# Kernel tuning notes

Measured on AMD Instinct MI355X. Metric: run time of the kernel, lower is better.

Reference implementation:

```python
import jax, jax.numpy as jnp
import numpy as np

GROUPS = 16
N_HEADS = 4
EPS = 1e-6


def setup_inputs() -> dict:
    key = jax.random.key(0)
    ks = jax.random.split(key, 7)
    N, C, D, H, W = 2, 256, 16, 16, 16
    x = jax.random.normal(ks[0], (N, C, D, H, W), jnp.float32)
    gn_scale = 1.0 + 0.02 * jax.random.normal(ks[1], (C,), jnp.float32)
    gn_bias = 0.02 * jax.random.normal(ks[2], (C,), jnp.float32)
    w_qkv = jax.random.normal(ks[3], (3 * C, C), jnp.float32) / np.sqrt(C).astype(np.float32)
    b_qkv = 0.02 * jax.random.normal(ks[4], (3 * C,), jnp.float32)
    # NOTE: original zero-inits w_out/b_out (zero_module); we use random values
    # so the kernel-correctness baseline is non-trivial. Same math.
    w_out = jax.random.normal(ks[5], (C, C), jnp.float32) / np.sqrt(C).astype(np.float32)
    b_out = 0.02 * jax.random.normal(ks[6], (C,), jnp.float32)
    return {"x": x, "gn_scale": gn_scale, "gn_bias": gn_bias,
            "w_qkv": w_qkv, "b_qkv": b_qkv, "w_out": w_out, "b_out": b_out}


def reference(x, gn_scale, gn_bias, w_qkv, b_qkv, w_out, b_out):
    N, C, D, H, W = x.shape
    L = D * H * W
    xf = x.reshape(N, C, L)
    # GroupNorm(16 groups, eps=1e-6, affine)
    xg = xf.reshape(N, GROUPS, C // GROUPS, L)
    mu = xg.mean(axis=(2, 3), keepdims=True)
    var = xg.var(axis=(2, 3), keepdims=True)
    xn = ((xg - mu) * jax.lax.rsqrt(var + EPS)).reshape(N, C, L)
    xn = xn * gn_scale[None, :, None] + gn_bias[None, :, None]
    # 1x1x1 Conv3d == channel matmul
    qkv = jnp.einsum('oc,ncl->nol', w_qkv, xn) + b_qkv[None, :, None]  # [N,3C,L]
    ch = C // N_HEADS
    qkv = qkv.reshape(N, 3, N_HEADS, ch, L)  # channel layout: (qkvs, head, ch)
    q, k, v = qkv[:, 0], qkv[:, 1], qkv[:, 2]  # each [N,heads,ch,L]
    scale = 1.0 / np.sqrt(np.sqrt(ch)).astype(np.float32)
    w = jnp.einsum('nhct,nhcs->nhts', q * scale, k * scale)  # [N,heads,L,L]
    w = jax.nn.softmax(w, axis=-1)
    a = jnp.einsum('nhts,nhcs->nhct', w, v).reshape(N, C, L)
    y = jnp.einsum('oc,ncl->nol', w_out, a) + b_out[None, :, None]
    return x + y.reshape(N, C, D, H, W)
```

## Files before the change

kernel.cpp:

```cpp
#include <hip/hip_runtime.h>

#define NB 2
#define CCH 256
#define LL 4096
#define NGRP 16
#define NHD 4
#define CHD 64
#define QR 768
#define SPLIT 4
#define TBLK 256

typedef __attribute__((ext_vector_type(8))) short short8;
typedef __attribute__((ext_vector_type(4))) float f32x4;
typedef __attribute__((ext_vector_type(4))) unsigned int uint32x4;

#define OFF_GP 64
#define OFF_BP 4224
#define OFF_WQ 5824
#define OFF_WO 202432
#define OFF_QT 235200
#define OFF_KT 1283776
#define OFF_V  2332352
#define OFF_PO 3380928
#define OFF_L  7575232
#define OFF_XT OFF_PO
#define OFF_AT OFF_QT

#define KSCALE 0.1803368801111204f

__device__ __forceinline__ unsigned short f2bf(float f) {
    unsigned int u = __builtin_bit_cast(unsigned int, f);
    u += 0x7fffu + ((u >> 16) & 1u);
    return (unsigned short)(u >> 16);
}
__device__ __forceinline__ float bf2f(unsigned short s) {
    unsigned int u = ((unsigned int)s) << 16;
    return __builtin_bit_cast(float, u);
}
__device__ __forceinline__ unsigned int cvtpk(float lo, float hi) {
    unsigned int r;
    asm("v_cvt_pk_bf16_f32 %0, %1, %2" : "=v"(r) : "v"(lo), "v"(hi));
    return r;
}

__device__ __forceinline__ short8 build_pf(const f32x4 s_lo, const f32x4 s_hi) {
    unsigned int a0 = cvtpk(s_lo[0], s_lo[1]);
    unsigned int b0 = cvtpk(s_hi[0], s_hi[1]);
    unsigned int a1 = cvtpk(s_lo[2], s_lo[3]);
    unsigned int b1 = cvtpk(s_hi[2], s_hi[3]);
    asm("v_permlane32_swap_b32 %0, %1" : "+v"(a0), "+v"(b0));
    asm("v_permlane16_swap_b32 %0, %1" : "+v"(a0), "+v"(b0));
    asm("v_permlane32_swap_b32 %0, %1" : "+v"(a1), "+v"(b1));
    asm("v_permlane16_swap_b32 %0, %1" : "+v"(a1), "+v"(b1));
    uint32x4 w = {a0, a1, b0, b1};
    return __builtin_bit_cast(short8, w);
}

__device__ __forceinline__ void stage_tile(unsigned short* lt,
                                           const unsigned short* src,
                                           int srcStride, int tid) {
    #pragma unroll
    for (int p = 0; p < 4; p++) {
        const int r  = p * 16 + (tid >> 4);
        const int cb = (tid & 15) * 2;
        const unsigned short* s = src + (size_t)r * srcStride + cb * 8;
        short8 a = *(const short8*)(s);
        short8 b = *(const short8*)(s + 8);
        char* d = (char*)lt + r * 512;
        *(short8*)(d + (((cb    ) ^ (r & 15)) << 4)) = a;
        *(short8*)(d + (((cb + 1) ^ (r & 15)) << 4)) = b;
    }
}
__device__ __forceinline__ short8 ldsfrag(const unsigned short* lt, int row, int ch) {
    return *(const short8*)((const char*)lt + row * 512 + ((ch ^ (row & 15)) << 4));
}

__global__ __launch_bounds__(256)
void k_xtgn(const float* __restrict__ x, unsigned short* __restrict__ xt,
            float* __restrict__ ws) {
    const int l0 = blockIdx.x * 64, c0 = blockIdx.y * 64, n = blockIdx.z;
    __shared__ __align__(16) unsigned short lt[64 * 64];
    __shared__ float red[2][4][4];
    const int tid = threadIdx.x;
    const int cl = tid >> 4;
    const int ll = (tid & 15) << 2;
    float s1[4], s2[4];
    #pragma unroll
    for (int cc = 0; cc < 4; cc++) {
        const int c = cl + cc * 16;
        float4 v = *(const float4*)(x + (size_t)(n * CCH + c0 + c) * LL + l0 + ll);
        s1[cc] = (v.x + v.y) + (v.z + v.w);
        s2[cc] = (v.x * v.x + v.y * v.y) + (v.z * v.z + v.w * v.w);
        const float vv[4] = {v.x, v.y, v.z, v.w};
        #pragma unroll
        for (int j = 0; j < 4; j++) {
            const int l = ll + j;
            const int byte = l * 128 + ((((c >> 3) ^ (l & 7)) << 4) | ((c & 7) * 2));
            *(unsigned short*)((char*)lt + byte) = f2bf(vv[j]);
        }
    }
    #pragma unroll
    for (int cc = 0; cc < 4; cc++)
        #pragma unroll
        for (int off = 32; off; off >>= 1) {
            s1[cc] += __shfl_down(s1[cc], off);
            s2[cc] += __shfl_down(s2[cc], off);
        }
    if ((tid & 63) == 0) {
        const int w = tid >> 6;
        #pragma unroll
        for (int cc = 0; cc < 4; cc++) { red[0][w][cc] = s1[cc]; red[1][w][cc] = s2[cc]; }
    }
    __syncthreads();
    if (tid < 4) {
        const float a = red[0][0][tid] + red[0][1][tid] + red[0][2][tid] + red[0][3][tid];
        const float b = red[1][0][tid] + red[1][1][tid] + red[1][2][tid] + red[1][3][tid];
        const int g = n * NGRP + (c0 >> 4) + tid;
        ws[OFF_GP + (g * 64 + blockIdx.x) * 2]     = a;
        ws[OFF_GP + (g * 64 + blockIdx.x) * 2 + 1] = b;
    }
    const int lr = tid >> 2;
    const int ch = (tid & 3) << 4;
    unsigned short* dst = xt + ((size_t)n * LL + l0 + lr) * CCH + c0 + ch;
    const int b0 = lr * 128 + ((((ch >> 3)    ) ^ (lr & 7)) << 4);
    const int b1 = lr * 128 + ((((ch >> 3) + 1) ^ (lr & 7)) << 4);
    *(short8*)dst       = *(const short8*)((char*)lt + b0);
    *(short8*)(dst + 8) = *(const short8*)((char*)lt + b1);
}

__device__ __forceinline__ void load_stats(const float* __restrict__ ws,
                                           float* smu, float* srs) {
    if (threadIdx.x < 32) {
        float s1 = 0.f, s2 = 0.f;
        #pragma unroll 8
        for (int i = 0; i < 64; i++) {
            s1 += ws[OFF_GP + (threadIdx.x * 64 + i) * 2];
            s2 += ws[OFF_GP + (threadIdx.x * 64 + i) * 2 + 1];
        }
        const float inv = 1.f / (float)(16 * LL);
        float m = s1 * inv;
        float var = s2 * inv - m * m;
        smu[threadIdx.x] = m;
        srs[threadIdx.x] = rsqrtf(var + 1e-6f);
    }
    __syncthreads();
}

__global__ __launch_bounds__(256)
void k_bpw(const float* __restrict__ w_qkv, const float* __restrict__ w_out,
           const float* __restrict__ b_qkv, const float* __restrict__ gn_scale,
           const float* __restrict__ gn_bias, float* __restrict__ ws,
           unsigned short* __restrict__ wq, unsigned short* __restrict__ wo) {
    __shared__ float smu[32], srs[32];
    load_stats(ws, smu, srs);
    if (blockIdx.x < 448) {
        const int e = (blockIdx.x * 256 + threadIdx.x) * 4;
        if (e < NB * QR * CCH) {
            const int n = (e >= QR * CCH) ? 1 : 0;
            const int r = e - n * QR * CCH;
            const int o = r >> 8, c = r & 255;
            float4 w  = *(const float4*)(w_qkv + (size_t)o * CCH + c);
            float4 gs = *(const float4*)(gn_scale + c);
            const float rs = srs[n * NGRP + (c >> 4)];
            const float sc = (o < 256 ? KSCALE : 1.0f) * rs;
            ushort4 u;
            u.x = f2bf(w.x * gs.x * sc); u.y = f2bf(w.y * gs.y * sc);
            u.z = f2bf(w.z * gs.z * sc); u.w = f2bf(w.w * gs.w * sc);
            *(ushort4*)(wq + (size_t)n * QR * CCH + r) = u;
        } else {
            const int r = e - NB * QR * CCH;
            float4 w = *(const float4*)(w_out + r);
            ushort4 u;
            u.x = f2bf(w.x); u.y = f2bf(w.y); u.z = f2bf(w.z); u.w = f2bf(w.w);
            *(ushort4*)(wo + r) = u;
        }
    } else {
        const int oi = (blockIdx.x - 448) * 32 + (threadIdx.x >> 3);
        const int j  = threadIdx.x & 7;
        const int n = (oi >= QR) ? 1 : 0;
        const int o = oi - n * QR;
        const float* wr = w_qkv + (size_t)o * CCH + j * 32;
        const float* gsr = gn_scale + j * 32;
        const float* gbr = gn_bias + j * 32;
        float s = 0.f;
        #pragma unroll
        for (int c = 0; c < 32; c += 4) {
            float4 w  = *(const float4*)(wr + c);
            float4 gs = *(const float4*)(gsr + c);
            float4 gb = *(const float4*)(gbr + c);
            const int gidx = n * NGRP + ((j * 32 + c) >> 4);
            const float mu = smu[gidx], rs = srs[gidx];
            s += w.x * (gb.x - mu * rs * gs.x) + w.y * (gb.y - mu * rs * gs.y)
               + w.z * (gb.z - mu * rs * gs.z) + w.w * (gb.w - mu * rs * gs.w);
        }
        s += __shfl_down(s, 4);
        s += __shfl_down(s, 2);
        s += __shfl_down(s, 1);
        if (j == 0) ws[OFF_BP + oi] = (b_qkv[o] + s) * (o < 256 ? KSCALE : 1.0f);
    }
}

__global__ __launch_bounds__(256)
void k_qkv(const unsigned short* __restrict__ wq, const float* __restrict__ bp,
           const unsigned short* __restrict__ xt,
           unsigned short* __restrict__ qT, unsigned short* __restrict__ kT,
           unsigned short* __restrict__ vv) {
    const int l0 = blockIdx.x * 64, o0 = blockIdx.y * 64, n = blockIdx.z;
    const int tid = threadIdx.x, w = tid >> 6, r16 = tid & 15, g = (tid & 63) >> 4;
    __shared__ __align__(16) unsigned short lt[64 * 256];
    const unsigned short* xb = xt + (size_t)n * LL * CCH;
    const unsigned short* wb = wq + (size_t)n * QR * CCH;
    const bool isv = (o0 >= 512);

    stage_tile(lt, isv ? (xb + (size_t)l0 * CCH) : (wb + (size_t)o0 * CCH), CCH, tid);
    __syncthreads();

    f32x4 acc[4];
    #pragma unroll
    for (int i = 0; i < 4; i++) acc[i] = (f32x4){0.f, 0.f, 0.f, 0.f};

    if (!isv) {
        const unsigned short* xr = xb + (size_t)(l0 + w * 16 + r16) * CCH + g * 8;
        for (int kk = 0; kk < 8; kk++) {
            short8 xf = *(const short8*)(xr + kk * 32);
            #pragma unroll
            for (int af = 0; af < 4; af++) {
                short8 wf = ldsfrag(lt, af * 16 + r16, kk * 4 + g);
                acc[af] = __builtin_amdgcn_mfma_f32_16x16x32_bf16(wf, xf, acc[af], 0, 0, 0);
            }
        }
        const bool isq = (o0 < 256);
        const int h = (o0 >> 6) & 3;
        unsigned short* tb = (isq ? qT : kT) + ((size_t)n * NHD + h) * LL * CHD;
        const int t = l0 + w * 16 + r16;
        #pragma unroll
        for (int af = 0; af < 4; af++) {
            float4 bb = *(const float4*)(bp + n * QR + o0 + af * 16 + g * 4);
            ushort4 u;
            u.x = f2bf(acc[af][0] + bb.x); u.y = f2bf(acc[af][1] + bb.y);
            u.z = f2bf(acc[af][2] + bb.z); u.w = f2bf(acc[af][3] + bb.w);
            *(ushort4*)(tb + (size_t)t * CHD + af * 16 + g * 4) = u;
        }
    } else {
        const unsigned short* wr = wb + (size_t)(o0 + w * 16 + r16) * CCH + g * 8;
        for (int kk = 0; kk < 8; kk++) {
            short8 wf = *(const short8*)(wr + kk * 32);
            #pragma unroll
            for (int lb = 0; lb < 4; lb++) {
                short8 xf = ldsfrag(lt, lb * 16 + r16, kk * 4 + g);
                acc[lb] = __builtin_amdgcn_mfma_f32_16x16x32_bf16(xf, wf, acc[lb], 0, 0, 0);
            }
        }
        const int h = (o0 - 512) >> 6;
        const int o = o0 + w * 16 + r16;
        const float bb = bp[n * QR + o];
        unsigned short* vb = vv + ((size_t)n * NHD + h) * CHD * LL + (size_t)(o & 63) * LL;
        #pragma unroll
        for (int lb = 0; lb < 4; lb++) {
            ushort4 u;
            u.x = f2bf(acc[lb][0] + bb); u.y = f2bf(acc[lb][1] + bb);
            u.z = f2bf(acc[lb][2] + bb); u.w = f2bf(acc[lb][3] + bb);
            *(ushort4*)(vb + l0 + lb * 16 + g * 4) = u;
        }
    }
}

__global__ __launch_bounds__(256, 2)
void k_attn(const unsigned short* __restrict__ qT,
            const unsigned short* __restrict__ kT,
            const unsigned short* __restrict__ vv,
            unsigned short* __restrict__ po, float* __restrict__ pl) {
    const int t0 = blockIdx.x * TBLK;
    const int h  = blockIdx.y;
    const int n  = blockIdx.z >> 2;
    const int sp = blockIdx.z & 3;
    const int tid = threadIdx.x;
    const int w = tid >> 6, l = tid & 63, r16 = l & 15, g = l >> 4;

    const size_t nh = (size_t)n * NHD + h;
    const unsigned short* qb = qT + nh * LL * CHD;
    const unsigned short* kb = kT + nh * LL * CHD;
    const unsigned short* vb = vv + nh * CHD * LL;
    const int s_beg = sp * (LL / SPLIT);

    __shared__ __align__(16) unsigned short kvs[2][2][64 * 64];

    const int srow = tid >> 2;
    const int ss0  = (tid & 3) << 1;
    const unsigned short* ksrc = kb + (size_t)(s_beg + srow) * CHD + ss0 * 8;
    const unsigned short* vsrc = vb + (size_t)srow * LL + s_beg + ss0 * 8;
    char* base0 = (char*)&kvs[0][0][0];
    const int kd0 = srow * 128 + (((ss0    ) ^ (srow & 7)) << 4);
    const int kd1 = srow * 128 + (((ss0 + 1) ^ (srow & 7)) << 4);

    const int tw = t0 + w * 64;
    const int jk0 = ((g    ) ^ (r16 & 7)) << 4;
    const int jk1 = ((4 + g) ^ (r16 & 7)) << 4;

    short8 qf[4][2];
    #pragma unroll
    for (int qg = 0; qg < 4; qg++) {
        const unsigned short* qr = qb + (size_t)(tw + qg * 16 + r16) * CHD + g * 8;
        qf[qg][0] = *(const short8*)(qr);
        qf[qg][1] = *(const short8*)(qr + 32);
    }

    f32x4 oacc[4][4];
    #pragma unroll
    for (int qg = 0; qg < 4; qg++)
        #pragma unroll
        for (int cb = 0; cb < 4; cb++) oacc[qg][cb] = (f32x4){0.f, 0.f, 0.f, 0.f};
    float lsum[4] = {0.f, 0.f, 0.f, 0.f};

    const int NIT = (LL / SPLIT) / 64;

    short8 kr0 = *(const short8*)(ksrc);
    short8 kr1 = *(const short8*)(ksrc + 8);
    short8 vr0 = *(const short8*)(vsrc);
    short8 vr1 = *(const short8*)(vsrc + 8);
    *(short8*)(base0 + kd0) = kr0;
    *(short8*)(base0 + kd1) = kr1;
    *(short8*)(base0 + 8192 + kd0) = vr0;
    *(short8*)(base0 + 8192 + kd1) = vr1;
    const unsigned short* kpf = ksrc + 64 * CHD;
    const unsigned short* vpf = vsrc + 64;
    kr0 = *(const short8*)(kpf);
    kr1 = *(const short8*)(kpf + 8);
    vr0 = *(const short8*)(vpf);
    vr1 = *(const short8*)(vpf + 8);
    __syncthreads();

    int cur = 0;
    for (int it = 0; it < NIT; it++) {
        const char* kB = base0 + cur * 16384;
        const char* vB = kB + 8192;

        short8 kf0[4], kf1[4];
        #pragma unroll
        for (int sb = 0; sb < 4; sb++) {
            const int rb = (16 * sb + r16) * 128;
            kf0[sb] = *(const short8*)(kB + rb + jk0);
            kf1[sb] = *(const short8*)(kB + rb + jk1);
        }
        if (it + 1 < NIT) {
            char* kdn = base0 + (cur ^ 1) * 16384;
            *(short8*)(kdn + kd0) = kr0;
            *(short8*)(kdn + kd1) = kr1;
            *(short8*)(kdn + 8192 + kd0) = vr0;
            *(short8*)(kdn + 8192 + kd1) = vr1;
        }
        if (it + 2 < NIT) {
            kpf += 64 * CHD;
            vpf += 64;
            kr0 = *(const short8*)(kpf);
            kr1 = *(const short8*)(kpf + 8);
            vr0 = *(const short8*)(vpf);
            vr1 = *(const short8*)(vpf + 8);
        }

        short8 pf[4][2];
        #pragma unroll
        for (int qg = 0; qg < 4; qg++) {
            f32x4 sa[4];
            #pragma unroll
            for (int sb = 0; sb < 4; sb++) {
                f32x4 z = (f32x4){0.f, 0.f, 0.f, 0.f};
                z = __builtin_amdgcn_mfma_f32_16x16x32_bf16(kf0[sb], qf[qg][0], z, 0, 0, 0);
                sa[sb] = __builtin_amdgcn_mfma_f32_16x16x32_bf16(kf1[sb], qf[qg][1], z, 0, 0, 0);
            }
            float rs0 = 0.f, rs1 = 0.f;
            #pragma unroll
            for (int sb = 0; sb < 4; sb++) {
                float p0 = __builtin_amdgcn_exp2f(sa[sb][0]);
                float p1 = __builtin_amdgcn_exp2f(sa[sb][1]);
                float p2 = __builtin_amdgcn_exp2f(sa[sb][2]);
                float p3 = __builtin_amdgcn_exp2f(sa[sb][3]);
                sa[sb][0] = p0; sa[sb][1] = p1;
                sa[sb][2] = p2; sa[sb][3] = p3;
                rs0 += p0 + p1;
                rs1 += p2 + p3;
            }
            lsum[qg] += rs0 + rs1;
            pf[qg][0] = build_pf(sa[0], sa[1]);
            pf[qg][1] = build_pf(sa[2], sa[3]);
        }

        __builtin_amdgcn_s_setprio(1);
        #pragma unroll
        for (int cb = 0; cb < 4; cb++) {
            const int rb = (16 * cb + r16) * 128;
            short8 vf0 = *(const short8*)(vB + rb + jk0);
            short8 vf1 = *(const short8*)(vB + rb + jk1);
            #pragma unroll
            for (int qg = 0; qg < 4; qg++) {
                oacc[qg][cb] = __builtin_amdgcn_mfma_f32_16x16x32_bf16(vf0, pf[qg][0], oacc[qg][cb], 0, 0, 0);
                oacc[qg][cb] = __builtin_amdgcn_mfma_f32_16x16x32_bf16(vf1, pf[qg][1], oacc[qg][cb], 0, 0, 0);
            }
        }
        __builtin_amdgcn_s_setprio(0);

        __syncthreads();
        cur ^= 1;
    }

    const size_t nhsp = ((size_t)sp * NB + n) * NHD + h;
    #pragma unroll
    for (int qg = 0; qg < 4; qg++) {
        float ls = lsum[qg];
        ls += __shfl_xor(ls, 16);
        ls += __shfl_xor(ls, 32);
        const int t = tw + qg * 16 + r16;
        unsigned short* pob = po + ((size_t)nhsp * LL + t) * CHD;
        #pragma unroll
        for (int cb = 0; cb < 4; cb++) {
            unsigned int lo = cvtpk(oacc[qg][cb][0], oacc[qg][cb][1]);
            unsigned int hi = cvtpk(oacc[qg][cb][2], oacc[qg][cb][3]);
            *(uint2*)(pob + cb * 16 + g * 4) = make_uint2(lo, hi);
        }
        if (g == 0) pl[nhsp * LL + t] = ls;
    }
}

__global__ __launch_bounds__(256)
void k_merge(const unsigned short* __restrict__ po, const float* __restrict__ pl,
             unsigned short* __restrict__ at) {
    const int idx = blockIdx.x * 256 + threadIdx.x;
    const int c16 = (idx & 3) << 4;
    const int t   = (idx >> 2) & (LL - 1);
    const int nh  = idx >> 14;
    float denom = 0.f;
    #pragma unroll
    for (int s = 0; s < SPLIT; s++)
        denom += pl[(size_t)(s * NB * NHD + nh) * LL + t];
    const float inv = 1.f / denom;
    float facc[16];
    #pragma unroll
    for (int k = 0; k < 16; k++) facc[k] = 0.f;
    #pragma unroll
    for (int s = 0; s < SPLIT; s++) {
        const unsigned short* pb = po + ((size_t)(s * NB * NHD + nh) * LL + t) * CHD + c16;
        short8 a = *(const short8*)(pb);
        short8 b = *(const short8*)(pb + 8);
        #pragma unroll
        for (int k = 0; k < 8; k++) {
            facc[k]     += bf2f((unsigned short)a[k]);
            facc[8 + k] += bf2f((unsigned short)b[k]);
        }
    }
    unsigned short* ob = at + ((size_t)(nh >> 2) * LL + t) * CCH + (nh & 3) * CHD + c16;
    #pragma unroll
    for (int q = 0; q < 4; q++) {
        ushort4 u;
        u.x = f2bf(facc[q * 4 + 0] * inv);
        u.y = f2bf(facc[q * 4 + 1] * inv);
        u.z = f2bf(facc[q * 4 + 2] * inv);
        u.w = f2bf(facc[q * 4 + 3] * inv);
        *(ushort4*)(ob + q * 4) = u;
    }
}

__global__ __launch_bounds__(256)
void k_out(const unsigned short* __restrict__ at, const unsigned short* __restrict__ wo,
           const float* __restrict__ b_out, const float* __restrict__ x,
           float* __restrict__ out) {
    const int l0 = blockIdx.x * 64, o0 = blockIdx.y * 64, n = blockIdx.z;
    const int tid = threadIdx.x, w = tid >> 6, r16 = tid & 15, g = (tid & 63) >> 4;
    __shared__ __align__(16) unsigned short lt[64 * 256];
    const unsigned short* ab = at + (size_t)n * LL * CCH;

    stage_tile(lt, ab + (size_t)l0 * CCH, CCH, tid);
    __syncthreads();

    const unsigned short* wr = wo + (size_t)(o0 + w * 16 + r16) * CCH + g * 8;
    f32x4 acc[4];
    #pragma unroll
    for (int i = 0; i < 4; i++) acc[i] = (f32x4){0.f, 0.f, 0.f, 0.f};
    for (int kk = 0; kk < 8; kk++) {
        short8 wf = *(const short8*)(wr + kk * 32);
        #pragma unroll
        for (int lb = 0; lb < 4; lb++) {
            short8 xf = ldsfrag(lt, lb * 16 + r16, kk * 4 + g);
            acc[lb] = __builtin_amdgcn_mfma_f32_16x16x32_bf16(xf, wf, acc[lb], 0, 0, 0);
        }
    }
    const int o = o0 + w * 16 + r16;
    const float bb = b_out[o];
    const float* xb = x + ((size_t)n * CCH + o) * LL;
    float* ob = out + ((size_t)n * CCH + o) * LL;
    #pragma unroll
    for (int lb = 0; lb < 4; lb++) {
        const int li = l0 + lb * 16 + g * 4;
        float4 xv = *(const float4*)(xb + li);
        float4 v;
        v.x = acc[lb][0] + bb + xv.x; v.y = acc[lb][1] + bb + xv.y;
        v.z = acc[lb][2] + bb + xv.z; v.w = acc[lb][3] + bb + xv.w;
        *(float4*)(ob + li) = v;
    }
}

extern "C" void kernel_launch(void* const* d_in, const int* in_sizes, int n_in,
                              void* d_out, int out_size, void* d_ws, size_t ws_size,
                              hipStream_t stream) {
    (void)in_sizes; (void)n_in; (void)out_size; (void)ws_size;
    const float* x        = (const float*)d_in[0];
    const float* gn_scale = (const float*)d_in[1];
    const float* gn_bias  = (const float*)d_in[2];
    const float* w_qkv    = (const float*)d_in[3];
    const float* b_qkv    = (const float*)d_in[4];
    const float* w_out    = (const float*)d_in[5];
    const float* b_out    = (const float*)d_in[6];
    float* out = (float*)d_out;
    float* ws  = (float*)d_ws;
    unsigned short* wq  = (unsigned short*)(ws + OFF_WQ);
    unsigned short* wo  = (unsigned short*)(ws + OFF_WO);
    unsigned short* xt  = (unsigned short*)(ws + OFF_XT);
    unsigned short* qT  = (unsigned short*)(ws + OFF_QT);
    unsigned short* kT  = (unsigned short*)(ws + OFF_KT);
    unsigned short* vv  = (unsigned short*)(ws + OFF_V);
    unsigned short* at  = (unsigned short*)(ws + OFF_AT);
    unsigned short* po  = (unsigned short*)(ws + OFF_PO);
    float* pl = ws + OFF_L;

    k_xtgn<<<dim3(64, 4, NB), 256, 0, stream>>>(x, xt, ws);
    k_bpw<<<dim3(496), 256, 0, stream>>>(w_qkv, w_out, b_qkv, gn_scale, gn_bias, ws, wq, wo);
    k_qkv<<<dim3(64, 12, NB), 256, 0, stream>>>(wq, ws + OFF_BP, xt, qT, kT, vv);
    k_attn<<<dim3(LL / TBLK, NHD, NB * SPLIT), 256, 0, stream>>>(qT, kT, vv, po, pl);
    k_merge<<<dim3(512), 256, 0, stream>>>(po, pl, at);
    k_out<<<dim3(64, 4, NB), 256, 0, stream>>>(at, wo, b_out, x, out);
}
```

Baseline: 80.26 us.

## Fuse split-merge into output projection and compute row sums via MFMA

Removes the separate merge kernel. The output-projection kernel now combines the split partial attention outputs, normalizes them, and stages the result in shared memory before the matmul, with each block handling 128 output channels. Softmax row sums are accumulated by an extra MFMA against a ones vector instead of VALU adds and cross-lane shuffles. The trade-off is that each partial-output tile is read by two blocks, and the denominator is now summed from bf16-rounded probabilities.

```diff
diff --git a/kernel.cpp b/kernel.cpp
--- a/kernel.cpp
+++ b/kernel.cpp
@@ -24,7 +24,6 @@
 #define OFF_PO 3380928
 #define OFF_L  7575232
 #define OFF_XT OFF_PO
-#define OFF_AT OFF_QT
 
 #define KSCALE 0.1803368801111204f
 
@@ -297,6 +296,10 @@
     const int jk0 = ((g    ) ^ (r16 & 7)) << 4;
     const int jk1 = ((4 + g) ^ (r16 & 7)) << 4;
 
+    short8 ones;
+    #pragma unroll
+    for (int i = 0; i < 8; i++) ones[i] = (short)0x3F80;
+
     short8 qf[4][2];
     #pragma unroll
     for (int qg = 0; qg < 4; qg++) {
@@ -305,12 +308,13 @@
         qf[qg][1] = *(const short8*)(qr + 32);
     }
 
-    f32x4 oacc[4][4];
-    #pragma unroll
-    for (int qg = 0; qg < 4; qg++)
+    f32x4 oacc[4][4], lacc[4];
+    #pragma unroll
+    for (int qg = 0; qg < 4; qg++) {
+        lacc[qg] = (f32x4){0.f, 0.f, 0.f, 0.f};
         #pragma unroll
         for (int cb = 0; cb < 4; cb++) oacc[qg][cb] = (f32x4){0.f, 0.f, 0.f, 0.f};
-    float lsum[4] = {0.f, 0.f, 0.f, 0.f};
+    }
 
     const int NIT = (LL / SPLIT) / 64;
 
@@ -368,19 +372,13 @@
                 z = __builtin_amdgcn_mfma_f32_16x16x32_bf16(kf0[sb], qf[qg][0], z, 0, 0, 0);
                 sa[sb] = __builtin_amdgcn_mfma_f32_16x16x32_bf16(kf1[sb], qf[qg][1], z, 0, 0, 0);
             }
-            float rs0 = 0.f, rs1 = 0.f;
             #pragma unroll
             for (int sb = 0; sb < 4; sb++) {
-                float p0 = __builtin_amdgcn_exp2f(sa[sb][0]);
-                float p1 = __builtin_amdgcn_exp2f(sa[sb][1]);
-                float p2 = __builtin_amdgcn_exp2f(sa[sb][2]);
-                float p3 = __builtin_amdgcn_exp2f(sa[sb][3]);
-                sa[sb][0] = p0; sa[sb][1] = p1;
-                sa[sb][2] = p2; sa[sb][3] = p3;
-                rs0 += p0 + p1;
-                rs1 += p2 + p3;
-            }
-            lsum[qg] += rs0 + rs1;
+                sa[sb][0] = __builtin_amdgcn_exp2f(sa[sb][0]);
+                sa[sb][1] = __builtin_amdgcn_exp2f(sa[sb][1]);
+                sa[sb][2] = __builtin_amdgcn_exp2f(sa[sb][2]);
+                sa[sb][3] = __builtin_amdgcn_exp2f(sa[sb][3]);
+            }
             pf[qg][0] = build_pf(sa[0], sa[1]);
             pf[qg][1] = build_pf(sa[2], sa[3]);
         }
@@ -397,6 +395,11 @@
                 oacc[qg][cb] = __builtin_amdgcn_mfma_f32_16x16x32_bf16(vf1, pf[qg][1], oacc[qg][cb], 0, 0, 0);
             }
         }
+        #pragma unroll
+        for (int qg = 0; qg < 4; qg++) {
+            lacc[qg] = __builtin_amdgcn_mfma_f32_16x16x32_bf16(ones, pf[qg][0], lacc[qg], 0, 0, 0);
+            lacc[qg] = __builtin_amdgcn_mfma_f32_16x16x32_bf16(ones, pf[qg][1], lacc[qg], 0, 0, 0);
+        }
         __builtin_amdgcn_s_setprio(0);
 
         __syncthreads();
@@ -406,9 +409,6 @@
     const size_t nhsp = ((size_t)sp * NB + n) * NHD + h;
     #pragma unroll
     for (int qg = 0; qg < 4; qg++) {
-        float ls = lsum[qg];
-        ls += __shfl_xor(ls, 16);
-        ls += __shfl_xor(ls, 32);
         const int t = tw + qg * 16 + r16;
         unsigned short* pob = po + ((size_t)nhsp * LL + t) * CHD;
         #pragma unroll
@@ -417,84 +417,87 @@
             unsigned int hi = cvtpk(oacc[qg][cb][2], oacc[qg][cb][3]);
             *(uint2*)(pob + cb * 16 + g * 4) = make_uint2(lo, hi);
         }
-        if (g == 0) pl[nhsp * LL + t] = ls;
+        if (g == 0) pl[nhsp * LL + t] = lacc[qg][0];
     }
 }
 
 __global__ __launch_bounds__(256)
-void k_merge(const unsigned short* __restrict__ po, const float* __restrict__ pl,
-             unsigned short* __restrict__ at) {
-    const int idx = blockIdx.x * 256 + threadIdx.x;
-    const int c16 = (idx & 3) << 4;
-    const int t   = (idx >> 2) & (LL - 1);
-    const int nh  = idx >> 14;
-    float denom = 0.f;
-    #pragma unroll
-    for (int s = 0; s < SPLIT; s++)
-        denom += pl[(size_t)(s * NB * NHD + nh) * LL + t];
-    const float inv = 1.f / denom;
-    float facc[16];
-    #pragma unroll
-    for (int k = 0; k < 16; k++) facc[k] = 0.f;
-    #pragma unroll
-    for (int s = 0; s < SPLIT; s++) {
-        const unsigned short* pb = po + ((size_t)(s * NB * NHD + nh) * LL + t) * CHD + c16;
-        short8 a = *(const short8*)(pb);
-        short8 b = *(const short8*)(pb + 8);
+void k_outm(const unsigned short* __restrict__ po, const float* __restrict__ pl,
+            const unsigned short* __restrict__ wo, const float* __restrict__ b_out,
+            const float* __restrict__ x, float* __restrict__ out) {
+    const int l0 = blockIdx.x * 64;
+    const int oh = blockIdx.y;
+    const int n  = blockIdx.z;
+    const int tid = threadIdx.x;
+    __shared__ __align__(16) unsigned short lt[64 * 256];
+
+    #pragma unroll
+    for (int p = 0; p < 4; p++) {
+        const int r  = p * 16 + (tid >> 4);
+        const int t  = l0 + r;
+        const int cb = (tid & 15) * 2;
+        const int c0 = cb * 8;
+        const int h  = c0 >> 6;
+        const int cc = c0 & 63;
+        float denom = 0.f;
+        float facc[16];
+        #pragma unroll
+        for (int k = 0; k < 16; k++) facc[k] = 0.f;
+        #pragma unroll
+        for (int s = 0; s < SPLIT; s++) {
+            const size_t idx = ((size_t)(s * NB + n) * NHD + h) * LL + t;
+            denom += pl[idx];
+            const unsigned short* pb = po + idx * CHD + cc;
+            short8 a = *(const short8*)(pb);
+            short8 b = *(const short8*)(pb + 8);
+            #pragma unroll
+            for (int k = 0; k < 8; k++) {
+                facc[k]     += bf2f((unsigned short)a[k]);
+                facc[8 + k] += bf2f((unsigned short)b[k]);
+            }
+        }
+        const float inv = 1.f / denom;
+        short8 s0, s1;
         #pragma unroll
         for (int k = 0; k < 8; k++) {
-            facc[k]     += bf2f((unsigned short)a[k]);
-            facc[8 + k] += bf2f((unsigned short)b[k]);
-        }
-    }
-    unsigned short* ob = at + ((size_t)(nh >> 2) * LL + t) * CCH + (nh & 3) * CHD + c16;
-    #pragma unroll
-    for (int q = 0; q < 4; q++) {
-        ushort4 u;
-        u.x = f2bf(facc[q * 4 + 0] * inv);
-        u.y = f2bf(facc[q * 4 + 1] * inv);
-        u.z = f2bf(facc[q * 4 + 2] * inv);
-        u.w = f2bf(facc[q * 4 + 3] * inv);
-        *(ushort4*)(ob + q * 4) = u;
-    }
-}
-
-__global__ __launch_bounds__(256)
-void k_out(const unsigned short* __restrict__ at, const unsigned short* __restrict__ wo,
-           const float* __restrict__ b_out, const float* __restrict__ x,
-           float* __restrict__ out) {
-    const int l0 = blockIdx.x * 64, o0 = blockIdx.y * 64, n = blockIdx.z;
-    const int tid = threadIdx.x, w = tid >> 6, r16 = tid & 15, g = (tid & 63) >> 4;
-    __shared__ __align__(16) unsigned short lt[64 * 256];
-    const unsigned short* ab = at + (size_t)n * LL * CCH;
-
-    stage_tile(lt, ab + (size_t)l0 * CCH, CCH, tid);
+            s0[k] = (short)f2bf(facc[k] * inv);
+            s1[k] = (short)f2bf(facc[8 + k] * inv);
+        }
+        char* d = (char*)lt + r * 512;
+        *(short8*)(d + (((cb    ) ^ (r & 15)) << 4)) = s0;
+        *(short8*)(d + (((cb + 1) ^ (r & 15)) << 4)) = s1;
+    }
     __syncthreads();
 
-    const unsigned short* wr = wo + (size_t)(o0 + w * 16 + r16) * CCH + g * 8;
-    f32x4 acc[4];
-    #pragma unroll
-    for (int i = 0; i < 4; i++) acc[i] = (f32x4){0.f, 0.f, 0.f, 0.f};
-    for (int kk = 0; kk < 8; kk++) {
-        short8 wf = *(const short8*)(wr + kk * 32);
+    const int w = tid >> 6, r16 = tid & 15, g = (tid & 63) >> 4;
+    #pragma unroll
+    for (int oi = 0; oi < 2; oi++) {
+        const int o0 = oh * 128 + oi * 64;
+        const unsigned short* wr = wo + (size_t)(o0 + w * 16 + r16) * CCH + g * 8;
+        f32x4 acc[4];
+        #pragma unroll
+        for (int i = 0; i < 4; i++) acc[i] = (f32x4){0.f, 0.f, 0.f, 0.f};
+        for (int kk = 0; kk < 8; kk++) {
+            short8 wf = *(const short8*)(wr + kk * 32);
+            #pragma unroll
+            for (int lb = 0; lb < 4; lb++) {
+                short8 xf = ldsfrag(lt, lb * 16 + r16, kk * 4 + g);
+                acc[lb] = __builtin_amdgcn_mfma_f32_16x16x32_bf16(xf, wf, acc[lb], 0, 0, 0);
+            }
+        }
+        const int o = o0 + w * 16 + r16;
+        const float bb = b_out[o];
+        const float* xb = x + ((size_t)n * CCH + o) * LL;
+        float* ob = out + ((size_t)n * CCH + o) * LL;
         #pragma unroll
         for (int lb = 0; lb < 4; lb++) {
-            short8 xf = ldsfrag(lt, lb * 16 + r16, kk * 4 + g);
-            acc[lb] = __builtin_amdgcn_mfma_f32_16x16x32_bf16(xf, wf, acc[lb], 0, 0, 0);
-        }
-    }
-    const int o = o0 + w * 16 + r16;
-    const float bb = b_out[o];
-    const float* xb = x + ((size_t)n * CCH + o) * LL;
-    float* ob = out + ((size_t)n * CCH + o) * LL;
-    #pragma unroll
-    for (int lb = 0; lb < 4; lb++) {
-        const int li = l0 + lb * 16 + g * 4;
-        float4 xv = *(const float4*)(xb + li);
-        float4 v;
-        v.x = acc[lb][0] + bb + xv.x; v.y = acc[lb][1] + bb + xv.y;
-        v.z = acc[lb][2] + bb + xv.z; v.w = acc[lb][3] + bb + xv.w;
-        *(float4*)(ob + li) = v;
+            const int li = l0 + lb * 16 + g * 4;
+            float4 xv = *(const float4*)(xb + li);
+            float4 v;
+            v.x = acc[lb][0] + bb + xv.x; v.y = acc[lb][1] + bb + xv.y;
+            v.z = acc[lb][2] + bb + xv.z; v.w = acc[lb][3] + bb + xv.w;
+            *(float4*)(ob + li) = v;
+        }
     }
 }
 
@@ -517,7 +520,6 @@
     unsigned short* qT  = (unsigned short*)(ws + OFF_QT);
     unsigned short* kT  = (unsigned short*)(ws + OFF_KT);
     unsigned short* vv  = (unsigned short*)(ws + OFF_V);
-    unsigned short* at  = (unsigned short*)(ws + OFF_AT);
     unsigned short* po  = (unsigned short*)(ws + OFF_PO);
     float* pl = ws + OFF_L;
 
@@ -525,6 +527,5 @@
     k_bpw<<<dim3(496), 256, 0, stream>>>(w_qkv, w_out, b_qkv, gn_scale, gn_bias, ws, wq, wo);
     k_qkv<<<dim3(64, 12, NB), 256, 0, stream>>>(wq, ws + OFF_BP, xt, qT, kT, vv);
     k_attn<<<dim3(LL / TBLK, NHD, NB * SPLIT), 256, 0, stream>>>(qT, kT, vv, po, pl);
-    k_merge<<<dim3(512), 256, 0, stream>>>(po, pl, at);
-    k_out<<<dim3(64, 4, NB), 256, 0, stream>>>(at, wo, b_out, x, out);
-}
+    k_outm<<<dim3(64, 2, NB), 256, 0, stream>>>(po, pl, wo, b_out, x, out);
+}
```

Result: no change. 81.44 us (+1.5%).

## Compute softmax row sums via MFMA with ones and use LDS-only barriers

Applied to the files above, without the earlier changes.

Replaces the scalar accumulation of exponentiated scores with an extra pair of MFMAs per query group that multiply the bf16 P fragments by a vector of ones, producing the row sums on the matrix cores. This removes VALU adds and the cross-lane shuffles at the end. It also swaps __syncthreads for a barrier that waits only on LDS counters, so global prefetch loads need not drain at each iteration. The sums are now taken from bf16-rounded P values, which changes numerics slightly, and the MFMA count per iteration rises.

```diff
diff --git a/kernel.cpp b/kernel.cpp
--- a/kernel.cpp
+++ b/kernel.cpp
@@ -41,6 +41,12 @@
     unsigned int r;
     asm("v_cvt_pk_bf16_f32 %0, %1, %2" : "=v"(r) : "v"(lo), "v"(hi));
     return r;
+}
+
+__device__ __forceinline__ void barrier_lds_only() {
+    asm volatile("s_waitcnt lgkmcnt(0)" ::: "memory");
+    __builtin_amdgcn_s_barrier();
+    __builtin_amdgcn_sched_barrier(0);
 }
 
 __device__ __forceinline__ short8 build_pf(const f32x4 s_lo, const f32x4 s_hi) {
@@ -297,6 +303,10 @@
     const int jk0 = ((g    ) ^ (r16 & 7)) << 4;
     const int jk1 = ((4 + g) ^ (r16 & 7)) << 4;
 
+    short8 ones;
+    #pragma unroll
+    for (int i = 0; i < 8; i++) ones[i] = (short)0x3F80;
+
     short8 qf[4][2];
     #pragma unroll
     for (int qg = 0; qg < 4; qg++) {
@@ -305,12 +315,13 @@
         qf[qg][1] = *(const short8*)(qr + 32);
     }
 
-    f32x4 oacc[4][4];
-    #pragma unroll
-    for (int qg = 0; qg < 4; qg++)
+    f32x4 oacc[4][4], lacc[4];
+    #pragma unroll
+    for (int qg = 0; qg < 4; qg++) {
+        lacc[qg] = (f32x4){0.f, 0.f, 0.f, 0.f};
         #pragma unroll
         for (int cb = 0; cb < 4; cb++) oacc[qg][cb] = (f32x4){0.f, 0.f, 0.f, 0.f};
-    float lsum[4] = {0.f, 0.f, 0.f, 0.f};
+    }
 
     const int NIT = (LL / SPLIT) / 64;
 
@@ -328,7 +339,7 @@
     kr1 = *(const short8*)(kpf + 8);
     vr0 = *(const short8*)(vpf);
     vr1 = *(const short8*)(vpf + 8);
-    __syncthreads();
+    barrier_lds_only();
 
     int cur = 0;
     for (int it = 0; it < NIT; it++) {
@@ -368,19 +379,13 @@
                 z = __builtin_amdgcn_mfma_f32_16x16x32_bf16(kf0[sb], qf[qg][0], z, 0, 0, 0);
                 sa[sb] = __builtin_amdgcn_mfma_f32_16x16x32_bf16(kf1[sb], qf[qg][1], z, 0, 0, 0);
             }
-            float rs0 = 0.f, rs1 = 0.f;
             #pragma unroll
             for (int sb = 0; sb < 4; sb++) {
-                float p0 = __builtin_amdgcn_exp2f(sa[sb][0]);
-                float p1 = __builtin_amdgcn_exp2f(sa[sb][1]);
-                float p2 = __builtin_amdgcn_exp2f(sa[sb][2]);
-                float p3 = __builtin_amdgcn_exp2f(sa[sb][3]);
-                sa[sb][0] = p0; sa[sb][1] = p1;
-                sa[sb][2] = p2; sa[sb][3] = p3;
-                rs0 += p0 + p1;
-                rs1 += p2 + p3;
+                sa[sb][0] = __builtin_amdgcn_exp2f(sa[sb][0]);
+                sa[sb][1] = __builtin_amdgcn_exp2f(sa[sb][1]);
+                sa[sb][2] = __builtin_amdgcn_exp2f(sa[sb][2]);
+                sa[sb][3] = __builtin_amdgcn_exp2f(sa[sb][3]);
             }
-            lsum[qg] += rs0 + rs1;
             pf[qg][0] = build_pf(sa[0], sa[1]);
             pf[qg][1] = build_pf(sa[2], sa[3]);
         }
@@ -397,18 +402,20 @@
                 oacc[qg][cb] = __builtin_amdgcn_mfma_f32_16x16x32_bf16(vf1, pf[qg][1], oacc[qg][cb], 0, 0, 0);
             }
         }
+        #pragma unroll
+        for (int qg = 0; qg < 4; qg++) {
+            lacc[qg] = __builtin_amdgcn_mfma_f32_16x16x32_bf16(ones, pf[qg][0], lacc[qg], 0, 0, 0);
+            lacc[qg] = __builtin_amdgcn_mfma_f32_16x16x32_bf16(ones, pf[qg][1], lacc[qg], 0, 0, 0);
+        }
         __builtin_amdgcn_s_setprio(0);
 
-        __syncthreads();
+        barrier_lds_only();
         cur ^= 1;
     }
 
     const size_t nhsp = ((size_t)sp * NB + n) * NHD + h;
     #pragma unroll
     for (int qg = 0; qg < 4; qg++) {
-        float ls = lsum[qg];
-        ls += __shfl_xor(ls, 16);
-        ls += __shfl_xor(ls, 32);
         const int t = tw + qg * 16 + r16;
         unsigned short* pob = po + ((size_t)nhsp * LL + t) * CHD;
         #pragma unroll
@@ -417,7 +424,7 @@
             unsigned int hi = cvtpk(oacc[qg][cb][2], oacc[qg][cb][3]);
             *(uint2*)(pob + cb * 16 + g * 4) = make_uint2(lo, hi);
         }
-        if (g == 0) pl[nhsp * LL + t] = ls;
+        if (g == 0) pl[nhsp * LL + t] = lacc[qg][0];
     }
 }
 
```

After: 79.22 us. About the same (-1.3%).
